# Kernel optimization log

Hardware: AMD Instinct MI355X
Metric: run time of the kernel (lower is better)

Reference implementation:

```python
import jax, jax.numpy as jnp
import numpy as np

SEQ_LEN, BSIZE, DIM_OBJ_QST = 128, 1024, 37
QST_DIM, HIDDEN, SLOTS = 11, 256, 20


def _linear_params(key, out_dim, in_dim):
    kw, kb = jax.random.split(key)
    # xavier_normal for weight, default uniform-ish small bias
    std = (2.0 / (in_dim + out_dim)) ** 0.5
    w = jax.random.normal(kw, (out_dim, in_dim), jnp.float32) * std
    b = jax.random.uniform(kb, (out_dim,), jnp.float32, -0.01, 0.01)
    return w, b


def setup_inputs() -> dict:
    key = jax.random.key(0)
    ks = jax.random.split(key, 10)
    memory_inputs = jax.random.normal(ks[0], (SEQ_LEN, BSIZE, DIM_OBJ_QST), jnp.float32)
    question_inputs = jax.random.normal(ks[1], (BSIZE, QST_DIM), jnp.float32)
    C_w, C_b = _linear_params(ks[2], HIDDEN, DIM_OBJ_QST)
    Q_w, Q_b = _linear_params(ks[3], HIDDEN, QST_DIM)
    H_w, H_b = _linear_params(ks[4], HIDDEN, 2 * HIDDEN)
    U_w, U_b = _linear_params(ks[5], HIDDEN, HIDDEN)
    V_w, V_b = _linear_params(ks[6], HIDDEN, HIDDEN)
    W_w, W_b = _linear_params(ks[7], HIDDEN, HIDDEN)
    J_w, J_b = _linear_params(ks[8], HIDDEN, 3 * HIDDEN)
    prelu_a = jnp.float32(1.0)  # nn.PReLU(init=1), single shared slope
    # nn.Embedding(num_mem_slots, hidden, padding_idx=0), uniform(-sqrt3, sqrt3), row 0 zeroed
    embed = jax.random.uniform(ks[9], (SLOTS, HIDDEN), jnp.float32, -(3.0 ** 0.5), 3.0 ** 0.5)
    embed = embed.at[0].set(0.0)
    return dict(memory_inputs=memory_inputs, question_inputs=question_inputs,
                C_w=C_w, C_b=C_b, Q_w=Q_w, Q_b=Q_b, H_w=H_w, H_b=H_b,
                U_w=U_w, U_b=U_b, V_w=V_w, V_b=V_b, W_w=W_w, W_b=W_b,
                J_w=J_w, J_b=J_b, prelu_a=prelu_a, embed=embed)


def reference(memory_inputs, question_inputs, C_w, C_b, Q_w, Q_b, H_w, H_b,
              U_w, U_b, V_w, V_b, W_w, W_b, J_w, J_b, prelu_a, embed):
    S, B, _ = memory_inputs.shape
    D, M = embed.shape[1], embed.shape[0]

    mi = jax.nn.relu(jnp.einsum('sbi,di->sbd', memory_inputs, C_w) + C_b)  # (S,B,D)
    q = jax.nn.relu(question_inputs @ Q_w.T + Q_b)                          # (B,D)

    # keys: embedding(arange(M)) tiled per batch, flattened to (B*M, D)
    keys = jnp.tile(embed[None, :, :], (B, 1, 1)).reshape(B * M, D)

    def step(memories, sentence):  # sentence: (B,D)
        sent = jnp.repeat(sentence, M, axis=0)                              # (B*M, D)
        gate = jax.nn.sigmoid(jnp.sum(sent * (memories + keys), axis=-1, keepdims=True))
        join = jnp.concatenate([memories @ U_w.T + U_b,
                                sent @ V_w.T + V_b,
                                keys @ W_w.T + W_b], axis=1)                # (B*M, 3D)
        j = jax.nn.relu(join) @ J_w.T + J_b
        cand = jnp.where(j > 0, j, prelu_a * j)                             # PReLU
        upd = memories + gate * cand
        upd = upd / (jnp.linalg.norm(upd, axis=-1, keepdims=True) + 1e-12)
        return upd, None

    memories, _ = jax.lax.scan(step, keys, mi)
    ng = memories.reshape(B, M, D)
    energies = jnp.sum(ng * q[:, None, :], axis=-1)                         # (B,M)
    attn = jax.nn.softmax(energies, axis=-1)
    attended = jnp.sum(ng * attn[:, :, None], axis=1)                       # (B,D)
    out = jax.nn.relu(jnp.concatenate([q, attended], axis=1) @ H_w.T + H_b)
    return out
```

## Files before the change

kernel.cpp:

```cpp
#include <hip/hip_runtime.h>
#include <hip/hip_bf16.h>


#define S_LEN 128
#define BSZ   1024
#define DOBJ  37
#define QD    11

typedef float f32x4 __attribute__((ext_vector_type(4)));
typedef short bf16x8 __attribute__((ext_vector_type(8)));
typedef short bf16x4 __attribute__((ext_vector_type(4)));

#define MFMA16(a, b, c) __builtin_amdgcn_mfma_f32_16x16x32_bf16((a), (b), (c), 0, 0, 0)

__device__ __forceinline__ float b2f(short h) {
    union { unsigned u; float f; } c; c.u = ((unsigned)(unsigned short)h) << 16; return c.f;
}
__device__ __forceinline__ short f2b(float x) {
    union { float f; unsigned u; } c; c.f = x;
    return (short)((c.u + 0x7FFFu + ((c.u >> 16) & 1u)) >> 16);
}
__device__ __forceinline__ unsigned pkbf(float a, float b) {
    union { __hip_bfloat162 h2; unsigned u; } c;
    c.h2 = __float22bfloat162_rn(make_float2(a, b));
    return c.u;
}
__device__ __forceinline__ float ld1(const void* p, int i, bool f32) {
    return f32 ? ((const float*)p)[i] : b2f(((const short*)p)[i]);
}
__device__ __forceinline__ bf16x8 ld8(const void* p, int i, bool f32) {
    if (!f32) return *(const bf16x8*)((const short*)p + i);
    const float* q = (const float*)p + i;
    bf16x8 r;
    #pragma unroll
    for (int e = 0; e < 8; ++e) r[e] = f2b(q[e]);
    return r;
}

__global__ __launch_bounds__(256, 2) void renet_phase1(
    const void* __restrict__ MI, const void* __restrict__ Cw, const void* __restrict__ Cb,
    const void* __restrict__ Vw, const void* __restrict__ Vb, const void* __restrict__ Jw,
    const void* __restrict__ PA, short* __restrict__ mi_out, short* __restrict__ jv_out)
{
    const bool F32 = (*(const unsigned*)PA == 0x3F800000u);
    __shared__ __align__(16) short A[64 * 264];
    __shared__ __align__(16) float MIL[64 * 40];
    __shared__ float VBL[256];

    const int t = threadIdx.x, r0 = blockIdx.x * 64;
    const int wv = t >> 6, lane = t & 63, lr = lane & 15, quad = lane >> 4;

    VBL[t] = ld1(Vb, t, F32);
    for (int c = 0; c < 10; ++c) {
        int idx = c * 256 + t;
        if (idx < 64 * 37) { int i = idx / 37, k = idx - i * 37; MIL[i * 40 + k] = ld1(MI, (r0 + i) * 37 + k, F32); }
    }
    __syncthreads();

    {
        float cw[DOBJ];
        #pragma unroll
        for (int k = 0; k < DOBJ; ++k) cw[k] = ld1(Cw, t * DOBJ + k, F32);
        float cb = ld1(Cb, t, F32);
        for (int i = 0; i < 64; ++i) {
            float a = cb;
            #pragma unroll
            for (int k = 0; k < DOBJ; ++k) a += MIL[i * 40 + k] * cw[k];
            short h = f2b(fmaxf(a, 0.f));
            A[i * 264 + t] = h;
            mi_out[(r0 + i) * 256 + t] = h;
        }
    }
    __syncthreads();

    const f32x4 Z4 = {0.f, 0.f, 0.f, 0.f};
    f32x4 acc[4][4];

    #pragma unroll
    for (int rt = 0; rt < 4; ++rt)
        #pragma unroll
        for (int nt = 0; nt < 4; ++nt) acc[rt][nt] = Z4;
    #pragma unroll
    for (int kt = 0; kt < 8; ++kt) {
        bf16x8 a[4];
        #pragma unroll
        for (int rt = 0; rt < 4; ++rt)
            a[rt] = *(const bf16x8*)&A[(rt * 16 + lr) * 264 + kt * 32 + quad * 8];
        #pragma unroll
        for (int nt = 0; nt < 4; ++nt) {
            int n = wv * 64 + nt * 16 + lr;
            bf16x8 b = ld8(Vw, n * 256 + kt * 32 + quad * 8, F32);
            #pragma unroll
            for (int rt = 0; rt < 4; ++rt) acc[rt][nt] = MFMA16(a[rt], b, acc[rt][nt]);
        }
    }
    __syncthreads();
    #pragma unroll
    for (int nt = 0; nt < 4; ++nt) {
        int n = wv * 64 + nt * 16 + lr;
        float vb = VBL[n];
        #pragma unroll
        for (int rt = 0; rt < 4; ++rt)
            #pragma unroll
            for (int r = 0; r < 4; ++r)
                A[(rt * 16 + quad * 4 + r) * 264 + n] = f2b(fmaxf(acc[rt][nt][r] + vb, 0.f));
    }
    __syncthreads();

    #pragma unroll
    for (int rt = 0; rt < 4; ++rt)
        #pragma unroll
        for (int nt = 0; nt < 4; ++nt) acc[rt][nt] = Z4;
    #pragma unroll
    for (int kt = 0; kt < 8; ++kt) {
        bf16x8 a[4];
        #pragma unroll
        for (int rt = 0; rt < 4; ++rt)
            a[rt] = *(const bf16x8*)&A[(rt * 16 + lr) * 264 + kt * 32 + quad * 8];
        #pragma unroll
        for (int nt = 0; nt < 4; ++nt) {
            int n = wv * 64 + nt * 16 + lr;
            bf16x8 b = ld8(Jw, n * 768 + 256 + kt * 32 + quad * 8, F32);
            #pragma unroll
            for (int rt = 0; rt < 4; ++rt) acc[rt][nt] = MFMA16(a[rt], b, acc[rt][nt]);
        }
    }
    __syncthreads();
    #pragma unroll
    for (int nt = 0; nt < 4; ++nt) {
        int n = wv * 64 + nt * 16 + lr;
        #pragma unroll
        for (int rt = 0; rt < 4; ++rt)
            #pragma unroll
            for (int r = 0; r < 4; ++r)
                A[(rt * 16 + quad * 4 + r) * 264 + n] = f2b(acc[rt][nt][r]);
    }
    __syncthreads();
    for (int c = 0; c < 16; ++c) {
        int idx = c * 1024 + t * 4;
        int i = idx >> 8, k = idx & 255;
        *(ushort4*)&jv_out[(r0 + i) * 256 + k] = *(const ushort4*)&A[i * 264 + k];
    }
}

__global__ __launch_bounds__(512, 2) void renet_recur(
    const short* __restrict__ mi, const short* __restrict__ jv,
    const void* __restrict__ Qin, const void* __restrict__ Qw, const void* __restrict__ Qb,
    const void* __restrict__ Uw, const void* __restrict__ Ub,
    const void* __restrict__ Jw, const void* __restrict__ Jb,
    const void* __restrict__ Ww, const void* __restrict__ Wb,
    const void* __restrict__ Hw, const void* __restrict__ Hb,
    const void* __restrict__ PA, const void* __restrict__ Emb, void* __restrict__ Out)
{
    const bool F32 = (*(const unsigned*)PA == 0x3F800000u);
    __shared__ __align__(16) short LDS[53856];
    short* const A1  = LDS;
    short* const STG = LDS + 26400;
    short* const SJ  = LDS + 47520;
    short* const JWL = LDS + 48576;

    const int t = threadIdx.x;
    const int w8 = t >> 6;
    const int lane = t & 63, lr = lane & 15, quad = lane >> 4;
    const int colb = w8 * 32;
    const float pa = ld1(PA, 0, F32);
    const f32x4 Z4 = {0.f, 0.f, 0.f, 0.f};
    const int bq0 = blockIdx.x * 4;

    float ub2[2][4];
    #pragma unroll
    for (int ct = 0; ct < 2; ++ct)
        #pragma unroll
        for (int r = 0; r < 4; ++r) ub2[ct][r] = ld1(Ub, colb + ct * 16 + quad * 4 + r, F32);

    bf16x8 uf[8][2], jf[8][2];
    #pragma unroll
    for (int kt = 0; kt < 8; ++kt)
        #pragma unroll
        for (int ct = 0; ct < 2; ++ct) {
            uf[kt][ct] = ld8(Uw, (colb + ct * 16 + lr) * 256 + kt * 32 + quad * 8, F32);
            jf[kt][ct] = ld8(Jw, (colb + ct * 16 + lr) * 768 + kt * 32 + quad * 8, F32);
        }

    for (int c = 0; c < 11; ++c) {
        int idx = c * 512 + t;
        if (idx < 20 * 264) {
            int row = idx / 264, k = idx - row * 264;
            A1[(80 + row) * 264 + k] = (k < 256) ? f2b(ld1(Emb, row * 256 + k, F32)) : (short)0;
        }
    }
    __syncthreads();

    {
        const int col = t & 255, grp = t >> 8, m0p = grp * 10;
        float* WKS = (float*)STG;
        float wacc[10];
        #pragma unroll
        for (int mm = 0; mm < 10; ++mm) wacc[mm] = 0.f;
        for (int c = 0; c < 32; ++c) {
            bf16x8 wv8 = ld8(Ww, col * 256 + c * 8, F32);
            float wf[8];
            #pragma unroll
            for (int e = 0; e < 8; ++e) wf[e] = b2f(wv8[e]);
            #pragma unroll
            for (int mm = 0; mm < 10; ++mm) {
                bf16x8 e8 = *(const bf16x8*)&A1[(80 + m0p + mm) * 264 + c * 8];
                float s = 0.f;
                #pragma unroll
                for (int e = 0; e < 8; ++e) s += b2f(e8[e]) * wf[e];
                wacc[mm] += s;
            }
        }
        float wb = ld1(Wb, col, F32);
        #pragma unroll
        for (int mm = 0; mm < 10; ++mm) WKS[(m0p + mm) * 256 + col] = fmaxf(wacc[mm] + wb, 0.f);
    }
    for (int c = 0; c < 42; ++c) {
        int idx = c * 512 + t;
        if (idx < 80 * 264) {
            int row = idx / 264, k = idx - row * 264;
            short v = (k < 256) ? A1[(80 + row % 20) * 264 + k] : (short)0;
            if (k == 256 || k == 257) v = (k == 257) ? (short)0x3F80 : (short)0;
            A1[idx] = v;
        }
    }
    __syncthreads();

    {
        const int col = t & 255, grp = t >> 8, m0p = grp * 10;
        const float* WKS = (const float*)STG;
        const float jb = ld1(Jb, col, F32);
        float jacc[10];
        #pragma unroll
        for (int mm = 0; mm < 10; ++mm) jacc[mm] = 0.f;
        for (int c = 0; c < 32; ++c) {
            bf16x8 j8 = ld8(Jw, col * 768 + 512 + c * 8, F32);
            float jfv[8];
            #pragma unroll
            for (int e = 0; e < 8; ++e) jfv[e] = b2f(j8[e]);
            #pragma unroll
            for (int mm = 0; mm < 10; ++mm) {
                float4 w0 = *(const float4*)&WKS[(m0p + mm) * 256 + c * 8];
                float4 w1 = *(const float4*)&WKS[(m0p + mm) * 256 + c * 8 + 4];
                jacc[mm] += w0.x * jfv[0] + w0.y * jfv[1] + w0.z * jfv[2] + w0.w * jfv[3]
                          + w1.x * jfv[4] + w1.y * jfv[5] + w1.z * jfv[6] + w1.w * jfv[7];
            }
        }
        #pragma unroll
        for (int mm = 0; mm < 10; ++mm) JWL[(m0p + mm) * 264 + col] = f2b(jacc[mm] + jb);
    }

    ushort4 pf_mi = {0, 0, 0, 0};
    if (t < 256) {
        pf_mi = *(const ushort4*)&mi[(bq0 + (t >> 6)) * 256 + (t & 63) * 4];
        *(ushort4*)&SJ[(t >> 6) * 264 + (t & 63) * 4] = pf_mi;
    }
    __syncthreads();

    for (int s = 0; s < S_LEN; ++s) {
        const int parO = (s & 1) << 1, parN = 2 - parO;

        if (s + 1 < S_LEN && t < 256)
            pf_mi = *(const ushort4*)&mi[((s + 1) * BSZ + bq0 + (t >> 6)) * 256 + (t & 63) * 4];

        float sc_o[5];
        #pragma unroll
        for (int nt = 0; nt < 5; ++nt)
            sc_o[nt] = 1.f / (sqrtf(*(const float*)&A1[(nt * 16 + lr) * 264 + 256 + parO]) + 1e-12f);

        if (w8 < 7) {
            const int base = (w8 < 5) ? w8 * 16 : (w8 == 5) ? 80 : 84;
            f32x4 ag = Z4;
            #pragma unroll
            for (int kt = 0; kt < 8; ++kt) {
                bf16x8 a = *(const bf16x8*)&SJ[lr * 264 + kt * 32 + quad * 8];
                bf16x8 b = *(const bf16x8*)&A1[(base + lr) * 264 + kt * 32 + quad * 8];
                ag = MFMA16(a, b, ag);
            }
            if (quad == 0) {
                const int row = base + lr;
                if (row < 80) {
                    const int bi = row / 20;
                    float sg = 1.f / (sqrtf(*(const float*)&A1[row * 264 + 256 + parO]) + 1e-12f);
                    float gm = (bi == 0) ? ag[0] : (bi == 1) ? ag[1] : (bi == 2) ? ag[2] : ag[3];
                    *(float*)&A1[row * 264 + 260] = gm * sg;
                } else {
                    float* gl = (float*)&A1[row * 264 + 256];
                    gl[0] = ag[0]; gl[1] = ag[1]; gl[2] = ag[2]; gl[3] = ag[3];
                }
            }
        }

        f32x4 acc[5][2];
        #pragma unroll
        for (int nt = 0; nt < 5; ++nt) { acc[nt][0] = Z4; acc[nt][1] = Z4; }
        #pragma unroll
        for (int kt = 0; kt < 8; ++kt) {
            bf16x8 b0 = *(const bf16x8*)&A1[( 0 + lr) * 264 + kt * 32 + quad * 8];
            bf16x8 b1 = *(const bf16x8*)&A1[(16 + lr) * 264 + kt * 32 + quad * 8];
            bf16x8 b2 = *(const bf16x8*)&A1[(32 + lr) * 264 + kt * 32 + quad * 8];
            bf16x8 b3 = *(const bf16x8*)&A1[(48 + lr) * 264 + kt * 32 + quad * 8];
            bf16x8 b4 = *(const bf16x8*)&A1[(64 + lr) * 264 + kt * 32 + quad * 8];
            acc[0][0] = MFMA16(uf[kt][0], b0, acc[0][0]);
            acc[1][0] = MFMA16(uf[kt][0], b1, acc[1][0]);
            acc[2][0] = MFMA16(uf[kt][0], b2, acc[2][0]);
            acc[3][0] = MFMA16(uf[kt][0], b3, acc[3][0]);
            acc[4][0] = MFMA16(uf[kt][0], b4, acc[4][0]);
            acc[0][1] = MFMA16(uf[kt][1], b0, acc[0][1]);
            acc[1][1] = MFMA16(uf[kt][1], b1, acc[1][1]);
            acc[2][1] = MFMA16(uf[kt][1], b2, acc[2][1]);
            acc[3][1] = MFMA16(uf[kt][1], b3, acc[3][1]);
            acc[4][1] = MFMA16(uf[kt][1], b4, acc[4][1]);
        }
        #pragma unroll
        for (int nt = 0; nt < 5; ++nt) {
            #pragma unroll
            for (int ct = 0; ct < 2; ++ct) {
                uint2 pk;
                pk.x = pkbf(fmaxf(acc[nt][ct][0] * sc_o[nt] + ub2[ct][0], 0.f),
                            fmaxf(acc[nt][ct][1] * sc_o[nt] + ub2[ct][1], 0.f));
                pk.y = pkbf(fmaxf(acc[nt][ct][2] * sc_o[nt] + ub2[ct][2], 0.f),
                            fmaxf(acc[nt][ct][3] * sc_o[nt] + ub2[ct][3], 0.f));
                *(uint2*)&STG[(nt * 16 + lr) * 264 + colb + ct * 16 + quad * 4] = pk;
            }
        }
        if (t < 80) *(float*)&A1[t * 264 + 256 + parN] = 0.f;
        __syncthreads();

        bf16x4 jvb0[2], jvb1[2], jvb2[2], jvb3[2];
        #pragma unroll
        for (int ct = 0; ct < 2; ++ct) {
            const int co = colb + ct * 16 + quad * 4;
            jvb0[ct] = *(const bf16x4*)&jv[(s * BSZ + bq0 + 0) * 256 + co];
            jvb1[ct] = *(const bf16x4*)&jv[(s * BSZ + bq0 + 1) * 256 + co];
            jvb2[ct] = *(const bf16x4*)&jv[(s * BSZ + bq0 + 2) * 256 + co];
            jvb3[ct] = *(const bf16x4*)&jv[(s * BSZ + bq0 + 3) * 256 + co];
        }

        f32x4 acc2[5][2];
        #pragma unroll
        for (int nt = 0; nt < 5; ++nt) { acc2[nt][0] = Z4; acc2[nt][1] = Z4; }
        #pragma unroll
        for (int kt = 0; kt < 8; ++kt) {
            bf16x8 b0 = *(const bf16x8*)&STG[( 0 + lr) * 264 + kt * 32 + quad * 8];
            bf16x8 b1 = *(const bf16x8*)&STG[(16 + lr) * 264 + kt * 32 + quad * 8];
            bf16x8 b2 = *(const bf16x8*)&STG[(32 + lr) * 264 + kt * 32 + quad * 8];
            bf16x8 b3 = *(const bf16x8*)&STG[(48 + lr) * 264 + kt * 32 + quad * 8];
            bf16x8 b4 = *(const bf16x8*)&STG[(64 + lr) * 264 + kt * 32 + quad * 8];
            acc2[0][0] = MFMA16(jf[kt][0], b0, acc2[0][0]);
            acc2[1][0] = MFMA16(jf[kt][0], b1, acc2[1][0]);
            acc2[2][0] = MFMA16(jf[kt][0], b2, acc2[2][0]);
            acc2[3][0] = MFMA16(jf[kt][0], b3, acc2[3][0]);
            acc2[4][0] = MFMA16(jf[kt][0], b4, acc2[4][0]);
            acc2[0][1] = MFMA16(jf[kt][1], b0, acc2[0][1]);
            acc2[1][1] = MFMA16(jf[kt][1], b1, acc2[1][1]);
            acc2[2][1] = MFMA16(jf[kt][1], b2, acc2[2][1]);
            acc2[3][1] = MFMA16(jf[kt][1], b3, acc2[3][1]);
            acc2[4][1] = MFMA16(jf[kt][1], b4, acc2[4][1]);
        }

        #pragma unroll
        for (int nt = 0; nt < 5; ++nt) {
            const int row = nt * 16 + lr;
            const int bi = row / 20;
            const int slot = row - bi * 20;
            float gp = *(const float*)&A1[row * 264 + 260]
                     + ((const float*)&A1[(80 + slot) * 264 + 256])[bi];
            float gate = 1.f / (1.f + __expf(-gp));
            float ss = 0.f;
            #pragma unroll
            for (int ct = 0; ct < 2; ++ct) {
                bf16x4 jw4  = *(const bf16x4*)&JWL[slot * 264 + colb + ct * 16 + quad * 4];
                bf16x4 old4 = *(const bf16x4*)&A1[row * 264 + colb + ct * 16 + quad * 4];
                bf16x4 jv4  = (bi == 0) ? jvb0[ct] : (bi == 1) ? jvb1[ct] : (bi == 2) ? jvb2[ct] : jvb3[ct];
                float u4[4];
                #pragma unroll
                for (int r = 0; r < 4; ++r) {
                    float j = acc2[nt][ct][r] + b2f(jv4[r]) + b2f(jw4[r]);
                    float cand = j > 0.f ? j : pa * j;
                    float u = b2f(old4[r]) * sc_o[nt] + gate * cand;
                    u4[r] = u;
                    ss += u * u;
                }
                uint2 pk;
                pk.x = pkbf(u4[0], u4[1]);
                pk.y = pkbf(u4[2], u4[3]);
                *(uint2*)&A1[row * 264 + colb + ct * 16 + quad * 4] = pk;
            }
            ss += __shfl_xor(ss, 16);
            ss += __shfl_xor(ss, 32);
            if (quad == 0)
                atomicAdd((float*)&A1[row * 264 + 256 + parN], ss);
        }
        if (t < 256) *(ushort4*)&SJ[(t >> 6) * 264 + (t & 63) * 4] = pf_mi;
        __syncthreads();
    }

    float* SF = (float*)STG;
    #pragma unroll
    for (int it = 0; it < 2; ++it) {
        const int idx = it * 512 + t, col = idx & 255, bi = idx >> 8;
        float a = ld1(Qb, col, F32);
        #pragma unroll
        for (int k = 0; k < QD; ++k)
            a += ld1(Qin, (bq0 + bi) * QD + k, F32) * ld1(Qw, col * QD + k, F32);
        SF[bi * 256 + col] = fmaxf(a, 0.f);
    }
    __syncthreads();
    if (t < 80) {
        int bi = t / 20;
        float e = 0.f;
        for (int c = 0; c < 32; ++c) {
            bf16x8 mv = *(const bf16x8*)&A1[t * 264 + c * 8];
            #pragma unroll
            for (int e8 = 0; e8 < 8; ++e8) e += b2f(mv[e8]) * SF[bi * 256 + c * 8 + e8];
        }
        float scf = 1.f / (sqrtf(*(const float*)&A1[t * 264 + 256]) + 1e-12f);
        SF[1024 + t] = e * scf;
    }
    __syncthreads();
    if (t < 4) {
        float mx = -1e30f;
        for (int m = 0; m < 20; ++m) mx = fmaxf(mx, SF[1024 + t * 20 + m]);
        float sm = 0.f, ex[20];
        for (int m = 0; m < 20; ++m) { ex[m] = __expf(SF[1024 + t * 20 + m] - mx); sm += ex[m]; }
        float inv = 1.f / sm;
        for (int m = 0; m < 20; ++m) {
            float scf = 1.f / (sqrtf(*(const float*)&A1[(t * 20 + m) * 264 + 256]) + 1e-12f);
            SF[1104 + t * 20 + m] = ex[m] * inv * scf;
        }
    }
    __syncthreads();
    #pragma unroll
    for (int it = 0; it < 2; ++it) {
        const int idx = it * 512 + t, col = idx & 255, bi = idx >> 8;
        float a = 0.f;
        for (int m = 0; m < 20; ++m)
            a += SF[1104 + bi * 20 + m] * b2f(A1[(bi * 20 + m) * 264 + col]);
        SF[1280 + bi * 512 + 256 + col] = a;
        SF[1280 + bi * 512 + col] = SF[bi * 256 + col];
    }
    __syncthreads();
    #pragma unroll
    for (int it = 0; it < 2; ++it) {
        const int idx = it * 512 + t, col = idx & 255, bi = idx >> 8;
        float o = ld1(Hb, col, F32);
        for (int c = 0; c < 64; ++c) {
            bf16x8 hv = ld8(Hw, col * 512 + c * 8, F32);
            #pragma unroll
            for (int e8 = 0; e8 < 8; ++e8) o += b2f(hv[e8]) * SF[1280 + bi * 512 + c * 8 + e8];
        }
        int oi = (bq0 + bi) * 256 + col;
        float v = fmaxf(o, 0.f);
        if (F32) ((float*)Out)[oi] = v; else ((short*)Out)[oi] = f2b(v);
    }
}

extern "C" void kernel_launch(void* const* d_in, const int* in_sizes, int n_in,
                              void* d_out, int out_size, void* d_ws, size_t ws_size,
                              hipStream_t stream) {
    (void)in_sizes; (void)n_in; (void)out_size; (void)ws_size;
    const void* MIp = d_in[0];
    const void* Qin = d_in[1];
    const void* Cw  = d_in[2];
    const void* Cb  = d_in[3];
    const void* Qw  = d_in[4];
    const void* Qb  = d_in[5];
    const void* Hw  = d_in[6];
    const void* Hb  = d_in[7];
    const void* Uw  = d_in[8];
    const void* Ub  = d_in[9];
    const void* Vw  = d_in[10];
    const void* Vb  = d_in[11];
    const void* Ww  = d_in[12];
    const void* Wb  = d_in[13];
    const void* Jw  = d_in[14];
    const void* Jb  = d_in[15];
    const void* PA  = d_in[16];
    const void* Emb = d_in[17];

    short* mi_ws = (short*)d_ws;
    short* jv_ws = mi_ws + (size_t)S_LEN * BSZ * 256;

    renet_phase1<<<dim3(2048), dim3(256), 0, stream>>>(MIp, Cw, Cb, Vw, Vb, Jw, PA, mi_ws, jv_ws);
    renet_recur<<<dim3(256), dim3(512), 0, stream>>>(mi_ws, jv_ws, Qin, Qw, Qb, Uw, Ub,
                                                     Jw, Jb, Ww, Wb, Hw, Hb, PA, Emb, d_out);
}
```

Before: 1.351 ms.

## Permute weight rows for 8-wide stores and fold gate MFMA into U loop

Permutes the U/J weight-fragment rows so each lane owns 8 contiguous output columns. Epilogue stores and loads then become 16-byte vectors instead of pairs of 8-byte ones, and the jv loads are hoisted to the top of the step so they overlap with compute. The per-row gate dot product for waves 0-4 now runs inside the U GEMM loop, reusing the already-loaded B fragments instead of a separate pass, and the second accumulator array is reused to cut register pressure. The cost is added branching inside the MFMA loop and a wave-dependent select.

```diff
diff --git a/kernel.cpp b/kernel.cpp
--- a/kernel.cpp
+++ b/kernel.cpp
@@ -163,23 +163,23 @@
     const int w8 = t >> 6;
     const int lane = t & 63, lr = lane & 15, quad = lane >> 4;
     const int colb = w8 * 32;
+    const int lcol = colb + quad * 8;
     const float pa = ld1(PA, 0, F32);
     const f32x4 Z4 = {0.f, 0.f, 0.f, 0.f};
     const int bq0 = blockIdx.x * 4;
 
-    float ub2[2][4];
-    #pragma unroll
-    for (int ct = 0; ct < 2; ++ct)
-        #pragma unroll
-        for (int r = 0; r < 4; ++r) ub2[ct][r] = ld1(Ub, colb + ct * 16 + quad * 4 + r, F32);
-
+    float ub8[8];
+    #pragma unroll
+    for (int c = 0; c < 8; ++c) ub8[c] = ld1(Ub, lcol + c, F32);
+
+    const int prow = colb + (lr >> 2) * 8 + (lr & 3);
     bf16x8 uf[8][2], jf[8][2];
     #pragma unroll
     for (int kt = 0; kt < 8; ++kt)
         #pragma unroll
         for (int ct = 0; ct < 2; ++ct) {
-            uf[kt][ct] = ld8(Uw, (colb + ct * 16 + lr) * 256 + kt * 32 + quad * 8, F32);
-            jf[kt][ct] = ld8(Jw, (colb + ct * 16 + lr) * 768 + kt * 32 + quad * 8, F32);
+            uf[kt][ct] = ld8(Uw, (prow + ct * 4) * 256 + kt * 32 + quad * 8, F32);
+            jf[kt][ct] = ld8(Jw, (prow + ct * 4) * 768 + kt * 32 + quad * 8, F32);
         }
 
     for (int c = 0; c < 11; ++c) {
@@ -263,13 +263,18 @@
         if (s + 1 < S_LEN && t < 256)
             pf_mi = *(const ushort4*)&mi[((s + 1) * BSZ + bq0 + (t >> 6)) * 256 + (t & 63) * 4];
 
+        const bf16x8 jva = *(const bf16x8*)&jv[(s * BSZ + bq0 + 0) * 256 + lcol];
+        const bf16x8 jvb = *(const bf16x8*)&jv[(s * BSZ + bq0 + 1) * 256 + lcol];
+        const bf16x8 jvc = *(const bf16x8*)&jv[(s * BSZ + bq0 + 2) * 256 + lcol];
+        const bf16x8 jvd = *(const bf16x8*)&jv[(s * BSZ + bq0 + 3) * 256 + lcol];
+
         float sc_o[5];
         #pragma unroll
         for (int nt = 0; nt < 5; ++nt)
             sc_o[nt] = 1.f / (sqrtf(*(const float*)&A1[(nt * 16 + lr) * 264 + 256 + parO]) + 1e-12f);
 
-        if (w8 < 7) {
-            const int base = (w8 < 5) ? w8 * 16 : (w8 == 5) ? 80 : 84;
+        if (w8 == 5 || w8 == 6) {
+            const int base = (w8 == 5) ? 80 : 84;
             f32x4 ag = Z4;
             #pragma unroll
             for (int kt = 0; kt < 8; ++kt) {
@@ -277,20 +282,10 @@
                 bf16x8 b = *(const bf16x8*)&A1[(base + lr) * 264 + kt * 32 + quad * 8];
                 ag = MFMA16(a, b, ag);
             }
-            if (quad == 0) {
-                const int row = base + lr;
-                if (row < 80) {
-                    const int bi = row / 20;
-                    float sg = 1.f / (sqrtf(*(const float*)&A1[row * 264 + 256 + parO]) + 1e-12f);
-                    float gm = (bi == 0) ? ag[0] : (bi == 1) ? ag[1] : (bi == 2) ? ag[2] : ag[3];
-                    *(float*)&A1[row * 264 + 260] = gm * sg;
-                } else {
-                    float* gl = (float*)&A1[row * 264 + 256];
-                    gl[0] = ag[0]; gl[1] = ag[1]; gl[2] = ag[2]; gl[3] = ag[3];
-                }
-            }
-        }
-
+            if (quad == 0) *(f32x4*)&A1[(base + lr) * 264 + 256] = ag;
+        }
+
+        f32x4 accg = Z4;
         f32x4 acc[5][2];
         #pragma unroll
         for (int nt = 0; nt < 5; ++nt) { acc[nt][0] = Z4; acc[nt][1] = Z4; }
@@ -301,6 +296,14 @@
             bf16x8 b2 = *(const bf16x8*)&A1[(32 + lr) * 264 + kt * 32 + quad * 8];
             bf16x8 b3 = *(const bf16x8*)&A1[(48 + lr) * 264 + kt * 32 + quad * 8];
             bf16x8 b4 = *(const bf16x8*)&A1[(64 + lr) * 264 + kt * 32 + quad * 8];
+            if (w8 < 5) {
+                bf16x8 sjf = *(const bf16x8*)&SJ[lr * 264 + kt * 32 + quad * 8];
+                if      (w8 == 0) accg = MFMA16(sjf, b0, accg);
+                else if (w8 == 1) accg = MFMA16(sjf, b1, accg);
+                else if (w8 == 2) accg = MFMA16(sjf, b2, accg);
+                else if (w8 == 3) accg = MFMA16(sjf, b3, accg);
+                else              accg = MFMA16(sjf, b4, accg);
+            }
             acc[0][0] = MFMA16(uf[kt][0], b0, acc[0][0]);
             acc[1][0] = MFMA16(uf[kt][0], b1, acc[1][0]);
             acc[2][0] = MFMA16(uf[kt][0], b2, acc[2][0]);
@@ -312,34 +315,30 @@
             acc[3][1] = MFMA16(uf[kt][1], b3, acc[3][1]);
             acc[4][1] = MFMA16(uf[kt][1], b4, acc[4][1]);
         }
+        if (w8 < 5 && quad == 0) {
+            const int row = w8 * 16 + lr;
+            const int bi = row / 20;
+            float g = (bi == 0) ? accg[0] : (bi == 1) ? accg[1] : (bi == 2) ? accg[2] : accg[3];
+            float scw = (w8 == 0) ? sc_o[0] : (w8 == 1) ? sc_o[1] : (w8 == 2) ? sc_o[2]
+                      : (w8 == 3) ? sc_o[3] : sc_o[4];
+            *(float*)&A1[row * 264 + 260] = g * scw;
+        }
         #pragma unroll
         for (int nt = 0; nt < 5; ++nt) {
-            #pragma unroll
-            for (int ct = 0; ct < 2; ++ct) {
-                uint2 pk;
-                pk.x = pkbf(fmaxf(acc[nt][ct][0] * sc_o[nt] + ub2[ct][0], 0.f),
-                            fmaxf(acc[nt][ct][1] * sc_o[nt] + ub2[ct][1], 0.f));
-                pk.y = pkbf(fmaxf(acc[nt][ct][2] * sc_o[nt] + ub2[ct][2], 0.f),
-                            fmaxf(acc[nt][ct][3] * sc_o[nt] + ub2[ct][3], 0.f));
-                *(uint2*)&STG[(nt * 16 + lr) * 264 + colb + ct * 16 + quad * 4] = pk;
-            }
+            float v[8];
+            #pragma unroll
+            for (int c = 0; c < 8; ++c)
+                v[c] = fmaxf(acc[nt][c >> 2][c & 3] * sc_o[nt] + ub8[c], 0.f);
+            uint4 pk;
+            pk.x = pkbf(v[0], v[1]); pk.y = pkbf(v[2], v[3]);
+            pk.z = pkbf(v[4], v[5]); pk.w = pkbf(v[6], v[7]);
+            *(uint4*)&STG[(nt * 16 + lr) * 264 + lcol] = pk;
         }
         if (t < 80) *(float*)&A1[t * 264 + 256 + parN] = 0.f;
         __syncthreads();
 
-        bf16x4 jvb0[2], jvb1[2], jvb2[2], jvb3[2];
-        #pragma unroll
-        for (int ct = 0; ct < 2; ++ct) {
-            const int co = colb + ct * 16 + quad * 4;
-            jvb0[ct] = *(const bf16x4*)&jv[(s * BSZ + bq0 + 0) * 256 + co];
-            jvb1[ct] = *(const bf16x4*)&jv[(s * BSZ + bq0 + 1) * 256 + co];
-            jvb2[ct] = *(const bf16x4*)&jv[(s * BSZ + bq0 + 2) * 256 + co];
-            jvb3[ct] = *(const bf16x4*)&jv[(s * BSZ + bq0 + 3) * 256 + co];
-        }
-
-        f32x4 acc2[5][2];
-        #pragma unroll
-        for (int nt = 0; nt < 5; ++nt) { acc2[nt][0] = Z4; acc2[nt][1] = Z4; }
+        #pragma unroll
+        for (int nt = 0; nt < 5; ++nt) { acc[nt][0] = Z4; acc[nt][1] = Z4; }
         #pragma unroll
         for (int kt = 0; kt < 8; ++kt) {
             bf16x8 b0 = *(const bf16x8*)&STG[( 0 + lr) * 264 + kt * 32 + quad * 8];
@@ -347,16 +346,16 @@
             bf16x8 b2 = *(const bf16x8*)&STG[(32 + lr) * 264 + kt * 32 + quad * 8];
             bf16x8 b3 = *(const bf16x8*)&STG[(48 + lr) * 264 + kt * 32 + quad * 8];
             bf16x8 b4 = *(const bf16x8*)&STG[(64 + lr) * 264 + kt * 32 + quad * 8];
-            acc2[0][0] = MFMA16(jf[kt][0], b0, acc2[0][0]);
-            acc2[1][0] = MFMA16(jf[kt][0], b1, acc2[1][0]);
-            acc2[2][0] = MFMA16(jf[kt][0], b2, acc2[2][0]);
-            acc2[3][0] = MFMA16(jf[kt][0], b3, acc2[3][0]);
-            acc2[4][0] = MFMA16(jf[kt][0], b4, acc2[4][0]);
-            acc2[0][1] = MFMA16(jf[kt][1], b0, acc2[0][1]);
-            acc2[1][1] = MFMA16(jf[kt][1], b1, acc2[1][1]);
-            acc2[2][1] = MFMA16(jf[kt][1], b2, acc2[2][1]);
-            acc2[3][1] = MFMA16(jf[kt][1], b3, acc2[3][1]);
-            acc2[4][1] = MFMA16(jf[kt][1], b4, acc2[4][1]);
+            acc[0][0] = MFMA16(jf[kt][0], b0, acc[0][0]);
+            acc[1][0] = MFMA16(jf[kt][0], b1, acc[1][0]);
+            acc[2][0] = MFMA16(jf[kt][0], b2, acc[2][0]);
+            acc[3][0] = MFMA16(jf[kt][0], b3, acc[3][0]);
+            acc[4][0] = MFMA16(jf[kt][0], b4, acc[4][0]);
+            acc[0][1] = MFMA16(jf[kt][1], b0, acc[0][1]);
+            acc[1][1] = MFMA16(jf[kt][1], b1, acc[1][1]);
+            acc[2][1] = MFMA16(jf[kt][1], b2, acc[2][1]);
+            acc[3][1] = MFMA16(jf[kt][1], b3, acc[3][1]);
+            acc[4][1] = MFMA16(jf[kt][1], b4, acc[4][1]);
         }
 
         #pragma unroll
@@ -367,26 +366,26 @@
             float gp = *(const float*)&A1[row * 264 + 260]
                      + ((const float*)&A1[(80 + slot) * 264 + 256])[bi];
             float gate = 1.f / (1.f + __expf(-gp));
-            float ss = 0.f;
-            #pragma unroll
-            for (int ct = 0; ct < 2; ++ct) {
-                bf16x4 jw4  = *(const bf16x4*)&JWL[slot * 264 + colb + ct * 16 + quad * 4];
-                bf16x4 old4 = *(const bf16x4*)&A1[row * 264 + colb + ct * 16 + quad * 4];
-                bf16x4 jv4  = (bi == 0) ? jvb0[ct] : (bi == 1) ? jvb1[ct] : (bi == 2) ? jvb2[ct] : jvb3[ct];
-                float u4[4];
-                #pragma unroll
-                for (int r = 0; r < 4; ++r) {
-                    float j = acc2[nt][ct][r] + b2f(jv4[r]) + b2f(jw4[r]);
-                    float cand = j > 0.f ? j : pa * j;
-                    float u = b2f(old4[r]) * sc_o[nt] + gate * cand;
-                    u4[r] = u;
-                    ss += u * u;
-                }
-                uint2 pk;
-                pk.x = pkbf(u4[0], u4[1]);
-                pk.y = pkbf(u4[2], u4[3]);
-                *(uint2*)&A1[row * 264 + colb + ct * 16 + quad * 4] = pk;
+            bf16x8 jw8  = *(const bf16x8*)&JWL[slot * 264 + lcol];
+            bf16x8 old8 = *(const bf16x8*)&A1[row * 264 + lcol];
+            bf16x8 jv8  = (nt == 0) ? jva
+                        : (nt == 1) ? ((lr < 4)  ? jva : jvb)
+                        : (nt == 2) ? ((lr < 8)  ? jvb : jvc)
+                        : (nt == 3) ? ((lr < 12) ? jvc : jvd)
+                        :             jvd;
+            float u8[8], ss = 0.f;
+            #pragma unroll
+            for (int c = 0; c < 8; ++c) {
+                float j = acc[nt][c >> 2][c & 3] + b2f(jv8[c]) + b2f(jw8[c]);
+                float cand = j > 0.f ? j : pa * j;
+                float u = b2f(old8[c]) * sc_o[nt] + gate * cand;
+                u8[c] = u;
+                ss += u * u;
             }
+            uint4 pk;
+            pk.x = pkbf(u8[0], u8[1]); pk.y = pkbf(u8[2], u8[3]);
+            pk.z = pkbf(u8[4], u8[5]); pk.w = pkbf(u8[6], u8[7]);
+            *(uint4*)&A1[row * 264 + lcol] = pk;
             ss += __shfl_xor(ss, 16);
             ss += __shfl_xor(ss, 32);
             if (quad == 0)
```

Result: slower. 1.528 ms (+13.2%).
